# Optimization experiments

Hardware: AMD Instinct MI355X
Metric: run time of the kernel (lower is better)

## Reference

```python
import jax, jax.numpy as jnp
import numpy as np

N_NODES = 100000
N_EDGES = 800000
IN_FEATS = 128
OUT_FEATS = 128
RANK_DIM = 128
NUM_BOND_TYPES = 32


def setup_inputs() -> dict:
    key = jax.random.key(0)
    ks = jax.random.split(key, 8)
    feat = jax.random.normal(ks[0], (N_NODES, IN_FEATS), dtype=jnp.float32)
    src = jax.random.randint(ks[1], (N_EDGES,), 0, N_NODES)
    dst = jax.random.randint(ks[2], (N_EDGES,), 0, N_NODES)
    # guarantee every node has in-degree >= 1 (module forbids 0-in-degree nodes)
    dst = dst.at[:N_NODES].set(jnp.arange(N_NODES))
    edge_attr = jax.random.randint(ks[3], (N_EDGES,), 0, NUM_BOND_TYPES)
    # xavier-uniform-like params
    def xavier(k, shape):
        lim = float(np.sqrt(6.0 / (shape[0] + shape[1])))
        return jax.random.uniform(k, shape, jnp.float32, -lim, lim)
    w1 = xavier(ks[4], (IN_FEATS, OUT_FEATS))
    w2 = xavier(ks[5], (IN_FEATS + 1, RANK_DIM))
    v = xavier(ks[6], (RANK_DIM, OUT_FEATS))
    bond_emb = jax.random.normal(ks[7], (NUM_BOND_TYPES, OUT_FEATS), dtype=jnp.float32)
    return {"feat": feat, "src": src, "dst": dst, "edge_attr": edge_attr,
            "w1": w1, "w2": w2, "v": v, "bond_emb": bond_emb}


def reference(feat, src, dst, edge_attr, w1, w2, v, bond_emb):
    N = feat.shape[0]
    E = src.shape[0]
    ones_e = jnp.ones((E,), dtype=feat.dtype)
    # norm == 'both': scale source features by out_degree^{-1/2}
    out_deg = jnp.clip(jax.ops.segment_sum(ones_e, src, num_segments=N), 1.0)
    feat_src = feat * (out_deg ** -0.5)[:, None]
    # two small GEMMs on node features
    h_sum = feat_src @ w1  # [N, out]
    feat_aug = jnp.concatenate([feat_src, jnp.ones((N, 1), dtype=feat.dtype)], axis=1)
    h_prod = jnp.tanh(feat_aug @ w2)  # [N, rank]
    # edge embedding (BondEncoder)
    ew = bond_emb[edge_attr]  # [E, out]
    # u_mul_e then neighbor-wise product / sum reductions onto dst
    m_prod = h_prod[src] * ew
    m_sum = h_sum[src] * ew
    hp = jax.ops.segment_prod(m_prod, dst, num_segments=N)
    hs = jax.ops.segment_sum(m_sum, dst, num_segments=N)
    rst = hs + hp @ v
    # norm == 'both': scale result by in_degree^{-1/2}
    in_deg = jnp.clip(jax.ops.segment_sum(ones_e, dst, num_segments=N), 1.0)
    rst = rst * (in_deg ** -0.5)[:, None]
    return rst
```

## Files before the change

### kernel.cpp

```cpp
#include <hip/hip_runtime.h>

#define N_NODES 100000
#define N_EDGES 800000

typedef unsigned short u16;
typedef unsigned int u32;
typedef __attribute__((ext_vector_type(8))) short short8;
typedef __attribute__((ext_vector_type(4))) float floatx4;

#define NBUK 196
#define BSH 9
#define NBLK 512
#define NE4 (N_EDGES / 4)
#define CE 391
#define NB_PREPW 192

__device__ __forceinline__ float bflo(u32 u) {
    union { u32 i; float f; } v; v.i = u << 16; return v.f;
}
__device__ __forceinline__ float bfhi(u32 u) {
    union { u32 i; float f; } v; v.i = u & 0xFFFF0000u; return v.f;
}
__device__ __forceinline__ u16 f2bf(float f) {
    union { float f; u32 i; } v; v.f = f;
    u32 r = (v.i + 0x7FFFu + ((v.i >> 16) & 1u)) >> 16;
    return (u16)r;
}
__device__ __forceinline__ float fast_tanh(float x) {
    float e = __expf(2.0f * x);
    return 1.0f - 2.0f * __builtin_amdgcn_rcpf(e + 1.0f);
}


__global__ __launch_bounds__(256) void kA_count(const int* __restrict__ src, const int* __restrict__ dst,
                                                int* __restrict__ countsD, int* __restrict__ countsS,
                                                const float* __restrict__ w1, const float* __restrict__ w2,
                                                const float* __restrict__ v, u16* __restrict__ wvfrag) {
    __shared__ int cd[NBUK], cs[NBUK];
    if (blockIdx.x >= NBLK) {
        int idx = (blockIdx.x - NBLK) * 256 + threadIdx.x;
        if (idx < 3 * 16384) {
            int m = idx >> 14, r = idx & 16383;
            int k = r >> 7, o = r & 127;
            float val = (m == 0) ? w1[k * 128 + o] : (m == 1) ? w2[k * 128 + o] : v[k * 128 + o];
            int ot = o >> 4, ks = k >> 5, quad = (k >> 3) & 3, j = k & 7;
            int lane = (quad << 4) | (o & 15);
            wvfrag[(((m * 8 + ot) * 4 + ks) * 64 + lane) * 8 + j] = f2bf(val);
        }
        return;
    }
    for (int i = threadIdx.x; i < NBUK; i += 256) { cd[i] = 0; cs[i] = 0; }
    __syncthreads();
    int i0 = blockIdx.x * CE;
    int i1 = i0 + CE; if (i1 > NE4) i1 = NE4;
    for (int i = i0 + threadIdx.x; i < i1; i += 256) {
        int4 d4 = ((const int4*)dst)[i];
        int4 s4 = ((const int4*)src)[i];
        atomicAdd(&cd[d4.x >> BSH], 1); atomicAdd(&cd[d4.y >> BSH], 1);
        atomicAdd(&cd[d4.z >> BSH], 1); atomicAdd(&cd[d4.w >> BSH], 1);
        atomicAdd(&cs[s4.x >> BSH], 1); atomicAdd(&cs[s4.y >> BSH], 1);
        atomicAdd(&cs[s4.z >> BSH], 1); atomicAdd(&cs[s4.w >> BSH], 1);
    }
    __syncthreads();
    for (int i = threadIdx.x; i < NBUK; i += 256) {
        countsD[i * NBLK + blockIdx.x] = cd[i];
        countsS[i * NBLK + blockIdx.x] = cs[i];
    }
}


__global__ __launch_bounds__(256) void kA_scan(int* __restrict__ countsD, int* __restrict__ countsS,
                                               int* __restrict__ totD, int* __restrict__ totS) {
    __shared__ int sc[256];
    int b = blockIdx.x;
    int* cnt = (b < NBUK) ? (countsD + b * NBLK) : (countsS + (b - NBUK) * NBLK);
    int t = threadIdx.x;
    int v0 = cnt[2 * t], v1 = cnt[2 * t + 1];
    int s = v0 + v1;
    sc[t] = s; __syncthreads();
    for (int off = 1; off < 256; off <<= 1) {
        int x = (t >= off) ? sc[t - off] : 0;
        __syncthreads();
        sc[t] += x;
        __syncthreads();
    }
    int excl = sc[t] - s;
    cnt[2 * t] = excl; cnt[2 * t + 1] = excl + v0;
    if (t == 255) { if (b < NBUK) totD[b] = sc[255]; else totS[b - NBUK] = sc[255]; }
}


__global__ __launch_bounds__(256) void kA_scatter(const int* __restrict__ src, const int* __restrict__ dst,
                                                  const int* __restrict__ attr,
                                                  const int* __restrict__ countsD, const int* __restrict__ countsS,
                                                  const int* __restrict__ totD, const int* __restrict__ totS,
                                                  uint2* __restrict__ dbuf, int* __restrict__ sbuf) {
    __shared__ int curD[NBUK], curS[NBUK];
    __shared__ int sd[256], ss[256];
    int t = threadIdx.x;
    int vd = (t < NBUK) ? totD[t] : 0;
    int vs = (t < NBUK) ? totS[t] : 0;
    sd[t] = vd; ss[t] = vs; __syncthreads();
    for (int off = 1; off < 256; off <<= 1) {
        int xd = (t >= off) ? sd[t - off] : 0;
        int xs = (t >= off) ? ss[t - off] : 0;
        __syncthreads();
        sd[t] += xd; ss[t] += xs;
        __syncthreads();
    }
    if (t < NBUK) {
        curD[t] = (sd[t] - vd) + countsD[t * NBLK + blockIdx.x];
        curS[t] = (ss[t] - vs) + countsS[t * NBLK + blockIdx.x];
    }
    __syncthreads();
    int i0 = blockIdx.x * CE;
    int i1 = i0 + CE; if (i1 > NE4) i1 = NE4;
    for (int i = i0 + t; i < i1; i += 256) {
        int4 s4 = ((const int4*)src)[i];
        int4 d4 = ((const int4*)dst)[i];
        int4 a4 = ((const int4*)attr)[i];
        int p, d, s, a;
        d = d4.x; s = s4.x; a = a4.x;
        p = atomicAdd(&curD[d >> BSH], 1); dbuf[p] = make_uint2((u32)d, (u32)((s << 5) | a));
        p = atomicAdd(&curS[s >> BSH], 1); sbuf[p] = s;
        d = d4.y; s = s4.y; a = a4.y;
        p = atomicAdd(&curD[d >> BSH], 1); dbuf[p] = make_uint2((u32)d, (u32)((s << 5) | a));
        p = atomicAdd(&curS[s >> BSH], 1); sbuf[p] = s;
        d = d4.z; s = s4.z; a = a4.z;
        p = atomicAdd(&curD[d >> BSH], 1); dbuf[p] = make_uint2((u32)d, (u32)((s << 5) | a));
        p = atomicAdd(&curS[s >> BSH], 1); sbuf[p] = s;
        d = d4.w; s = s4.w; a = a4.w;
        p = atomicAdd(&curD[d >> BSH], 1); dbuf[p] = make_uint2((u32)d, (u32)((s << 5) | a));
        p = atomicAdd(&curS[s >> BSH], 1); sbuf[p] = s;
    }
}


__global__ __launch_bounds__(256) void k_build(const uint2* __restrict__ dbuf, const int* __restrict__ sbuf,
                                               const int* __restrict__ totD, const int* __restrict__ totS,
                                               int* __restrict__ csr_start, int* __restrict__ in_deg,
                                               float* __restrict__ in_scale, float* __restrict__ out_scale,
                                               int* __restrict__ csr_edge) {
    __shared__ int cnt[512];
    __shared__ int aux[512];
    __shared__ int sc[256];
    __shared__ int sbase;
    int t = threadIdx.x;
    int isS = blockIdx.x >= NBUK;
    int b = isS ? (blockIdx.x - NBUK) : blockIdx.x;
    const int* tot = isS ? totS : totD;
    if (t < 64) {
        int s = 0;
        for (int i = t; i < b; i += 64) s += tot[i];
#pragma unroll
        for (int o = 32; o > 0; o >>= 1) s += __shfl_down(s, o);
        if (t == 0) sbase = s;
    }
    for (int i = t; i < 512; i += 256) cnt[i] = 0;
    __syncthreads();
    int st = sbase, n = tot[b];
    int nb0 = b << BSH;
    if (isS) {
        for (int i = st + t; i < st + n; i += 256) atomicAdd(&cnt[sbuf[i] - nb0], 1);
        __syncthreads();
        for (int s2 = t; s2 < 512; s2 += 256) {
            int node = nb0 + s2;
            if (node < N_NODES) { int c = cnt[s2]; if (c < 1) c = 1; out_scale[node] = rsqrtf((float)c); }
        }
        return;
    }
    for (int i = st + t; i < st + n; i += 256) { uint2 r = dbuf[i]; atomicAdd(&cnt[(int)r.x - nb0], 1); }
    __syncthreads();
    int c0 = cnt[2 * t], c1 = cnt[2 * t + 1];
    int s = c0 + c1; sc[t] = s; __syncthreads();
    for (int off = 1; off < 256; off <<= 1) {
        int x = (t >= off) ? sc[t - off] : 0;
        __syncthreads();
        sc[t] += x;
        __syncthreads();
    }
    int excl = sc[t] - s;
    aux[2 * t] = excl; aux[2 * t + 1] = excl + c0;
    int na = nb0 + 2 * t, nbv = nb0 + 2 * t + 1;
    if (na < N_NODES) {
        in_deg[na] = c0; int cc = c0 < 1 ? 1 : c0;
        in_scale[na] = rsqrtf((float)cc); csr_start[na] = st + excl;
    }
    if (nbv < N_NODES) {
        in_deg[nbv] = c1; int cc = c1 < 1 ? 1 : c1;
        in_scale[nbv] = rsqrtf((float)cc); csr_start[nbv] = st + excl + c0;
    }
    __syncthreads();
    for (int i = st + t; i < st + n; i += 256) {
        uint2 r = dbuf[i];
        int pos = atomicAdd(&aux[(int)r.x - nb0], 1);
        csr_edge[st + pos] = (int)r.y;
    }
}


__global__ __launch_bounds__(256) void k_gemm(const float* __restrict__ feat,
                                              const float* __restrict__ out_scale,
                                              const u16* __restrict__ wvfrag,
                                              const float* __restrict__ w2,
                                              u16* __restrict__ hrow) {
    int wave = threadIdx.x >> 6, lane = threadIdx.x & 63;
    int quad = lane >> 4, l15 = lane & 15;
    const float* bias = w2 + 128 * 128;
    float bias_v[8];
#pragma unroll
    for (int ot = 0; ot < 8; ot++) bias_v[ot] = bias[ot * 16 + l15];
    const short8* wv = (const short8*)wvfrag;
    int nb = blockIdx.x * 64 + wave * 16;
    int anode = nb + l15; if (anode >= N_NODES) anode = N_NODES - 1;
    float s = out_scale[anode];
    short8 a[4];
#pragma unroll
    for (int ks = 0; ks < 4; ks++) {
        float4 f0 = *(const float4*)(feat + anode * 128 + ks * 32 + quad * 8);
        float4 f1 = *(const float4*)(feat + anode * 128 + ks * 32 + quad * 8 + 4);
        short8 av;
        av[0] = (short)f2bf(f0.x * s); av[1] = (short)f2bf(f0.y * s);
        av[2] = (short)f2bf(f0.z * s); av[3] = (short)f2bf(f0.w * s);
        av[4] = (short)f2bf(f1.x * s); av[5] = (short)f2bf(f1.y * s);
        av[6] = (short)f2bf(f1.z * s); av[7] = (short)f2bf(f1.w * s);
        a[ks] = av;
    }
#pragma unroll
    for (int ot = 0; ot < 8; ot++) {
        floatx4 accS = (floatx4){0.f, 0.f, 0.f, 0.f};
        floatx4 accP = (floatx4){0.f, 0.f, 0.f, 0.f};
#pragma unroll
        for (int ks = 0; ks < 4; ks++) {
            short8 b0 = wv[(ot * 4 + ks) * 64 + lane];
            short8 b1 = wv[((8 + ot) * 4 + ks) * 64 + lane];
            accS = __builtin_amdgcn_mfma_f32_16x16x32_bf16(a[ks], b0, accS, 0, 0, 0);
            accP = __builtin_amdgcn_mfma_f32_16x16x32_bf16(a[ks], b1, accP, 0, 0, 0);
        }
        int o = ot * 16 + l15;
#pragma unroll
        for (int r = 0; r < 4; r++) {
            int node = nb + quad * 4 + r;
            if (node < N_NODES) {
                u32 pv = (u32)f2bf(accS[r]) | ((u32)f2bf(fast_tanh(accP[r] + bias_v[ot])) << 16);
                *(u32*)(hrow + node * 256 + o * 2) = pv;
            }
        }
    }
}


__global__ __launch_bounds__(256, 8) void k_edge(const int* __restrict__ csr_start, const int* __restrict__ in_deg,
                                                 const int* __restrict__ csr_edge,
                                                 const u16* __restrict__ hrow,
                                                 const float* __restrict__ bond_emb,
                                                 float* __restrict__ out_hs, u16* __restrict__ hp) {
    int wid = (blockIdx.x * 256 + threadIdx.x) >> 6;
    int lane = threadIdx.x & 63;
    int nwaves = (gridDim.x * 256) >> 6;
    const int NPAIR = N_NODES / 2;
    uint2 hC0 = {0, 0}, hC1 = {0, 0};
    float2 eC0 = {0.f, 0.f}, eC1 = {0.f, 0.f};
    for (int pr = wid; pr < NPAIR; pr += nwaves) {
        int n0 = pr * 2, n1 = n0 + 1;
        int st0 = csr_start[n0];
        int2 dd = *(const int2*)(in_deg + n0);
        int d0 = dd.x, d1 = dd.y;
        int st1 = st0 + d0;
        float as0 = 0.f, as1 = 0.f, ap0 = 1.f, ap1 = 1.f;
        float bs0 = 0.f, bs1 = 0.f, bp0 = 1.f, bp1 = 1.f;
        int b0 = 0, b1 = 0;
        while (b0 < d0 || b1 < d1) {
            int c0 = d0 - b0; c0 = c0 < 0 ? 0 : (c0 > 64 ? 64 : c0);
            int c1 = d1 - b1; c1 = c1 < 0 ? 0 : (c1 > 64 ? 64 : c1);
            int pkv0 = 0, pkv1 = 0;
            if (c0 > 0) { int li = lane < c0 ? lane : c0 - 1; pkv0 = csr_edge[st0 + b0 + li]; }
            if (c1 > 0) { int li = lane < c1 ? lane : c1 - 1; pkv1 = csr_edge[st1 + b1 + li]; }
            uint2 hA0 = hC0, hB0 = hC0, hA1 = hC1, hB1 = hC1;
            float2 eA0 = eC0, eB0 = eC0, eA1 = eC1, eB1 = eC1;
            if (c0 > 0) {
                int pk = __builtin_amdgcn_readlane(pkv0, 0);
                hA0 = *(const uint2*)(hrow + (pk >> 5) * 256 + 4 * lane);
                eA0 = *(const float2*)(bond_emb + (pk & 31) * 128 + 2 * lane);
                if (c0 > 1) {
                    pk = __builtin_amdgcn_readlane(pkv0, 1);
                    hB0 = *(const uint2*)(hrow + (pk >> 5) * 256 + 4 * lane);
                    eB0 = *(const float2*)(bond_emb + (pk & 31) * 128 + 2 * lane);
                }
            }
            if (c1 > 0) {
                int pk = __builtin_amdgcn_readlane(pkv1, 0);
                hA1 = *(const uint2*)(hrow + (pk >> 5) * 256 + 4 * lane);
                eA1 = *(const float2*)(bond_emb + (pk & 31) * 128 + 2 * lane);
                if (c1 > 1) {
                    pk = __builtin_amdgcn_readlane(pkv1, 1);
                    hB1 = *(const uint2*)(hrow + (pk >> 5) * 256 + 4 * lane);
                    eB1 = *(const float2*)(bond_emb + (pk & 31) * 128 + 2 * lane);
                }
            }
            int cm = c0 > c1 ? c0 : c1;
            for (int j = 0; j < cm; j++) {
                int jn = j + 2;
                if (jn < c0) {
                    int pk = __builtin_amdgcn_readlane(pkv0, jn);
                    hC0 = *(const uint2*)(hrow + (pk >> 5) * 256 + 4 * lane);
                    eC0 = *(const float2*)(bond_emb + (pk & 31) * 128 + 2 * lane);
                }
                if (jn < c1) {
                    int pk = __builtin_amdgcn_readlane(pkv1, jn);
                    hC1 = *(const uint2*)(hrow + (pk >> 5) * 256 + 4 * lane);
                    eC1 = *(const float2*)(bond_emb + (pk & 31) * 128 + 2 * lane);
                }
                if (j < c0) {
                    as0 += bflo(hA0.x) * eA0.x;
                    ap0 *= bfhi(hA0.x) * eA0.x;
                    as1 += bflo(hA0.y) * eA0.y;
                    ap1 *= bfhi(hA0.y) * eA0.y;
                    hA0 = hB0; eA0 = eB0; hB0 = hC0; eB0 = eC0;
                }
                if (j < c1) {
                    bs0 += bflo(hA1.x) * eA1.x;
                    bp0 *= bfhi(hA1.x) * eA1.x;
                    bs1 += bflo(hA1.y) * eA1.y;
                    bp1 *= bfhi(hA1.y) * eA1.y;
                    hA1 = hB1; eA1 = eB1; hB1 = hC1; eB1 = eC1;
                }
            }
            b0 += 64; b1 += 64;
        }
        float2 sv0; sv0.x = as0; sv0.y = as1;
        float2 sv1; sv1.x = bs0; sv1.y = bs1;
        *(float2*)(out_hs + n0 * 128 + 2 * lane) = sv0;
        *(float2*)(out_hs + n1 * 128 + 2 * lane) = sv1;
        *(u32*)(hp + n0 * 128 + 2 * lane) = ((u32)f2bf(ap1) << 16) | (u32)f2bf(ap0);
        *(u32*)(hp + n1 * 128 + 2 * lane) = ((u32)f2bf(bp1) << 16) | (u32)f2bf(bp0);
    }
}


__global__ __launch_bounds__(256) void k_final(const u16* __restrict__ hp,
                                               const u16* __restrict__ vfrag,
                                               const float* __restrict__ in_scale,
                                               float* __restrict__ out) {
    int wave = threadIdx.x >> 6, lane = threadIdx.x & 63;
    int quad = lane >> 4, l15 = lane & 15;
    const short8* wv = (const short8*)vfrag;
    int nb = blockIdx.x * 64 + wave * 16;
    int anode = nb + l15; if (anode >= N_NODES) anode = N_NODES - 1;
    short8 a[4];
#pragma unroll
    for (int ks = 0; ks < 4; ks++)
        a[ks] = *(const short8*)(hp + anode * 128 + ks * 32 + quad * 8);
#pragma unroll
    for (int ot = 0; ot < 8; ot++) {
        floatx4 acc = (floatx4){0.f, 0.f, 0.f, 0.f};
#pragma unroll
        for (int ks = 0; ks < 4; ks++) {
            short8 b = wv[(ot * 4 + ks) * 64 + lane];
            acc = __builtin_amdgcn_mfma_f32_16x16x32_bf16(a[ks], b, acc, 0, 0, 0);
        }
        int o = ot * 16 + l15;
#pragma unroll
        for (int r = 0; r < 4; r++) {
            int node = nb + quad * 4 + r;
            if (node < N_NODES) {
                float scl = in_scale[node];
                float hsv = out[node * 128 + o];
                out[node * 128 + o] = (acc[r] + hsv) * scl;
            }
        }
    }
}

extern "C" void kernel_launch(void* const* d_in, const int* in_sizes, int n_in,
                              void* d_out, int out_size, void* d_ws, size_t ws_size,
                              hipStream_t stream) {
    const float* feat = (const float*)d_in[0];
    const int* src = (const int*)d_in[1];
    const int* dst = (const int*)d_in[2];
    const int* attr = (const int*)d_in[3];
    const float* w1 = (const float*)d_in[4];
    const float* w2 = (const float*)d_in[5];
    const float* v = (const float*)d_in[6];
    const float* bond = (const float*)d_in[7];
    float* out = (float*)d_out;

    char* ws = (char*)d_ws;
    size_t off = 0;
    auto alloc = [&](size_t bytes) -> char* {
        char* p = ws + off; off += (bytes + 255) & ~(size_t)255; return p;
    };
    int* countsD   = (int*)alloc((size_t)NBUK * NBLK * 4);
    int* countsS   = (int*)alloc((size_t)NBUK * NBLK * 4);
    int* totD      = (int*)alloc((size_t)NBUK * 4);
    int* totS      = (int*)alloc((size_t)NBUK * 4);
    uint2* dbuf    = (uint2*)alloc((size_t)N_EDGES * 8);
    int* sbuf      = (int*)alloc((size_t)N_EDGES * 4);
    int* csr_start = (int*)alloc((size_t)N_NODES * 4);
    int* in_deg    = (int*)alloc((size_t)N_NODES * 4);
    float* out_scale = (float*)alloc((size_t)N_NODES * 4);
    float* in_scale  = (float*)alloc((size_t)N_NODES * 4);
    int* csr_edge  = (int*)alloc((size_t)N_EDGES * 4);
    u16* wvfrag = (u16*)alloc((size_t)3 * 16384 * 2);
    u16* hrow   = (u16*)alloc((size_t)N_NODES * 256 * 2);
    u16* hp     = (u16*)alloc((size_t)N_NODES * 128 * 2);

    (void)in_sizes; (void)n_in; (void)out_size; (void)ws_size;

    kA_count<<<NBLK + NB_PREPW, 256, 0, stream>>>(src, dst, countsD, countsS, w1, w2, v, wvfrag);
    kA_scan<<<2 * NBUK, 256, 0, stream>>>(countsD, countsS, totD, totS);
    kA_scatter<<<NBLK, 256, 0, stream>>>(src, dst, attr, countsD, countsS, totD, totS, dbuf, sbuf);
    k_build<<<2 * NBUK, 256, 0, stream>>>(dbuf, sbuf, totD, totS,
                                          csr_start, in_deg, in_scale, out_scale, csr_edge);
    k_gemm<<<(N_NODES + 63) / 64, 256, 0, stream>>>(feat, out_scale, wvfrag, w2, hrow);
    k_edge<<<2048, 256, 0, stream>>>(csr_start, in_deg, csr_edge, hrow, bond, out, hp);
    k_final<<<(N_NODES + 63) / 64, 256, 0, stream>>>(hp, wvfrag + 2 * 16384, in_scale, out);
}
```

Baseline: 268.8 us.

## Pack bucket-sort records into 32/16-bit words and halve partition block count

Edge records in the bucketed sort are packed: the destination's low 9 bits, the source and the bond type share one 32-bit word, and the source buffer stores only a 16-bit local offset. This halves the bytes written by the scatter and read by the CSR build. The partition/scatter block count is also halved (256 blocks, each covering twice as many edges), so the per-bucket scan becomes one element per thread and the count arrays shrink. Fewer blocks mean less parallelism in the count and scatter kernels.

Measured after the change: 265.1 us. About the same (-1.4%).

```diff
diff --git a/kernel.cpp b/kernel.cpp
--- a/kernel.cpp
+++ b/kernel.cpp
@@ -10,9 +10,9 @@
 
 #define NBUK 196
 #define BSH 9
-#define NBLK 512
+#define NBLK 256
 #define NE4 (N_EDGES / 4)
-#define CE 391
+#define CE 782
 #define NB_PREPW 192
 
 __device__ __forceinline__ float bflo(u32 u) {
@@ -75,17 +75,15 @@
     int b = blockIdx.x;
     int* cnt = (b < NBUK) ? (countsD + b * NBLK) : (countsS + (b - NBUK) * NBLK);
     int t = threadIdx.x;
-    int v0 = cnt[2 * t], v1 = cnt[2 * t + 1];
-    int s = v0 + v1;
-    sc[t] = s; __syncthreads();
+    int v0 = cnt[t];
+    sc[t] = v0; __syncthreads();
     for (int off = 1; off < 256; off <<= 1) {
         int x = (t >= off) ? sc[t - off] : 0;
         __syncthreads();
         sc[t] += x;
         __syncthreads();
     }
-    int excl = sc[t] - s;
-    cnt[2 * t] = excl; cnt[2 * t + 1] = excl + v0;
+    cnt[t] = sc[t] - v0;
     if (t == 255) { if (b < NBUK) totD[b] = sc[255]; else totS[b - NBUK] = sc[255]; }
 }
 
@@ -94,7 +92,7 @@
                                                   const int* __restrict__ attr,
                                                   const int* __restrict__ countsD, const int* __restrict__ countsS,
                                                   const int* __restrict__ totD, const int* __restrict__ totS,
-                                                  uint2* __restrict__ dbuf, int* __restrict__ sbuf) {
+                                                  u32* __restrict__ dbuf, u16* __restrict__ sbuf) {
     __shared__ int curD[NBUK], curS[NBUK];
     __shared__ int sd[256], ss[256];
     int t = threadIdx.x;
@@ -121,22 +119,26 @@
         int4 a4 = ((const int4*)attr)[i];
         int p, d, s, a;
         d = d4.x; s = s4.x; a = a4.x;
-        p = atomicAdd(&curD[d >> BSH], 1); dbuf[p] = make_uint2((u32)d, (u32)((s << 5) | a));
-        p = atomicAdd(&curS[s >> BSH], 1); sbuf[p] = s;
+        p = atomicAdd(&curD[d >> BSH], 1);
+        dbuf[p] = ((u32)(d & 511) << 22) | ((u32)s << 5) | (u32)a;
+        p = atomicAdd(&curS[s >> BSH], 1); sbuf[p] = (u16)(s & 511);
         d = d4.y; s = s4.y; a = a4.y;
-        p = atomicAdd(&curD[d >> BSH], 1); dbuf[p] = make_uint2((u32)d, (u32)((s << 5) | a));
-        p = atomicAdd(&curS[s >> BSH], 1); sbuf[p] = s;
+        p = atomicAdd(&curD[d >> BSH], 1);
+        dbuf[p] = ((u32)(d & 511) << 22) | ((u32)s << 5) | (u32)a;
+        p = atomicAdd(&curS[s >> BSH], 1); sbuf[p] = (u16)(s & 511);
         d = d4.z; s = s4.z; a = a4.z;
-        p = atomicAdd(&curD[d >> BSH], 1); dbuf[p] = make_uint2((u32)d, (u32)((s << 5) | a));
-        p = atomicAdd(&curS[s >> BSH], 1); sbuf[p] = s;
+        p = atomicAdd(&curD[d >> BSH], 1);
+        dbuf[p] = ((u32)(d & 511) << 22) | ((u32)s << 5) | (u32)a;
+        p = atomicAdd(&curS[s >> BSH], 1); sbuf[p] = (u16)(s & 511);
         d = d4.w; s = s4.w; a = a4.w;
-        p = atomicAdd(&curD[d >> BSH], 1); dbuf[p] = make_uint2((u32)d, (u32)((s << 5) | a));
-        p = atomicAdd(&curS[s >> BSH], 1); sbuf[p] = s;
-    }
-}
-
-
-__global__ __launch_bounds__(256) void k_build(const uint2* __restrict__ dbuf, const int* __restrict__ sbuf,
+        p = atomicAdd(&curD[d >> BSH], 1);
+        dbuf[p] = ((u32)(d & 511) << 22) | ((u32)s << 5) | (u32)a;
+        p = atomicAdd(&curS[s >> BSH], 1); sbuf[p] = (u16)(s & 511);
+    }
+}
+
+
+__global__ __launch_bounds__(256) void k_build(const u32* __restrict__ dbuf, const u16* __restrict__ sbuf,
                                                const int* __restrict__ totD, const int* __restrict__ totS,
                                                int* __restrict__ csr_start, int* __restrict__ in_deg,
                                                float* __restrict__ in_scale, float* __restrict__ out_scale,
@@ -161,7 +163,7 @@
     int st = sbase, n = tot[b];
     int nb0 = b << BSH;
     if (isS) {
-        for (int i = st + t; i < st + n; i += 256) atomicAdd(&cnt[sbuf[i] - nb0], 1);
+        for (int i = st + t; i < st + n; i += 256) atomicAdd(&cnt[sbuf[i]], 1);
         __syncthreads();
         for (int s2 = t; s2 < 512; s2 += 256) {
             int node = nb0 + s2;
@@ -169,7 +171,7 @@
         }
         return;
     }
-    for (int i = st + t; i < st + n; i += 256) { uint2 r = dbuf[i]; atomicAdd(&cnt[(int)r.x - nb0], 1); }
+    for (int i = st + t; i < st + n; i += 256) { u32 r = dbuf[i]; atomicAdd(&cnt[r >> 22], 1); }
     __syncthreads();
     int c0 = cnt[2 * t], c1 = cnt[2 * t + 1];
     int s = c0 + c1; sc[t] = s; __syncthreads();
@@ -192,9 +194,9 @@
     }
     __syncthreads();
     for (int i = st + t; i < st + n; i += 256) {
-        uint2 r = dbuf[i];
-        int pos = atomicAdd(&aux[(int)r.x - nb0], 1);
-        csr_edge[st + pos] = (int)r.y;
+        u32 r = dbuf[i];
+        int pos = atomicAdd(&aux[r >> 22], 1);
+        csr_edge[st + pos] = (int)(r & 0x3FFFFFu);
     }
 }
 
@@ -394,8 +396,8 @@
     int* countsS   = (int*)alloc((size_t)NBUK * NBLK * 4);
     int* totD      = (int*)alloc((size_t)NBUK * 4);
     int* totS      = (int*)alloc((size_t)NBUK * 4);
-    uint2* dbuf    = (uint2*)alloc((size_t)N_EDGES * 8);
-    int* sbuf      = (int*)alloc((size_t)N_EDGES * 4);
+    u32* dbuf      = (u32*)alloc((size_t)N_EDGES * 4);
+    u16* sbuf      = (u16*)alloc((size_t)N_EDGES * 2);
     int* csr_start = (int*)alloc((size_t)N_NODES * 4);
     int* in_deg    = (int*)alloc((size_t)N_NODES * 4);
     float* out_scale = (float*)alloc((size_t)N_NODES * 4);
```
